# Performance work log

Hardware: AMD Instinct MI355X
Metric: run time of the kernel (lower is better)

## Reference

```python
import jax, jax.numpy as jnp
import numpy as np

B, T, C = 2, 2048, 1024
H, D = 16, 64
F = 4096
EPS = 1e-5


def _layernorm(x, scale, shift):
    mean = jnp.mean(x, axis=-1, keepdims=True)
    var = jnp.mean((x - mean) ** 2, axis=-1, keepdims=True)  # unbiased=False
    return scale * (x - mean) * jax.lax.rsqrt(var + EPS) + shift


def setup_inputs() -> dict:
    key = jax.random.key(0)
    ks = jax.random.split(key, 16)
    s = lambda k, shape, fan_in: jax.random.normal(k, shape, jnp.float32) * (1.0 / np.sqrt(fan_in))
    return {
        "x": jax.random.normal(ks[0], (B, T, C), jnp.float32),
        # weights stored [in, out] so y = x @ W + b (same math as torch Linear)
        "Wq": s(ks[1], (C, H * D), C), "bq": jnp.zeros((H * D,), jnp.float32),
        "Wk": s(ks[2], (C, H * D), C), "bk": jnp.zeros((H * D,), jnp.float32),
        "Wv": s(ks[3], (C, H * D), C), "bv": jnp.zeros((H * D,), jnp.float32),
        "Wo": s(ks[4], (H * D, C), H * D), "bo": jnp.zeros((C,), jnp.float32),
        "W1": s(ks[5], (C, F), C), "b1": jnp.zeros((F,), jnp.float32),
        "W2": s(ks[6], (F, C), F), "b2": jnp.zeros((C,), jnp.float32),
        "ln1_scale": jnp.ones((C,), jnp.float32), "ln1_shift": jnp.zeros((C,), jnp.float32),
        "ln2_scale": jnp.ones((C,), jnp.float32), "ln2_shift": jnp.zeros((C,), jnp.float32),
    }


def reference(x, Wq, bq, Wk, bk, Wv, bv, Wo, bo, W1, b1, W2, b2,
              ln1_scale, ln1_shift, ln2_scale, ln2_shift):
    b, t, c = x.shape
    # --- attention sub-block ---
    h = _layernorm(x, ln1_scale, ln1_shift)
    q = (h @ Wq + bq).reshape(b, t, H, D)
    k = (h @ Wk + bk).reshape(b, t, H, D)
    v = (h @ Wv + bv).reshape(b, t, H, D)
    scores = jnp.einsum('bqhd,bkhd->bhqk', q, k)  # [B,H,T,T]
    causal = jnp.tril(jnp.ones((t, t), dtype=bool))
    scores = jnp.where(causal, scores, -jnp.inf)
    attn = jax.nn.softmax(scores / np.sqrt(D), axis=-1)
    ctx = jnp.einsum('bhqk,bkhd->bqhd', attn, v).reshape(b, t, H * D)
    x = x + (ctx @ Wo + bo)  # drop_rate=0 -> dropout is identity
    # --- MLP sub-block ---
    h = _layernorm(x, ln2_scale, ln2_shift)
    h = jax.nn.gelu(h @ W1 + b1, approximate=False)
    x = x + (h @ W2 + b2)
    return x
```

## Files before the change

### kernel.cpp

```cpp
#include <hip/hip_runtime.h>
#include <hip/hip_bf16.h>
#include <stdint.h>

#define B_ 2
#define T_ 2048
#define C_ 1024
#define H_ 16
#define D_ 64
#define F_ 4096
#define M_ (B_*T_)

typedef unsigned short ushort_t;
typedef __attribute__((ext_vector_type(8))) short short8;
typedef __attribute__((ext_vector_type(4))) float f32x4;

__device__ __forceinline__ float bf2f(ushort_t u) {
    union { unsigned u; float f; } c; c.u = ((unsigned)u) << 16; return c.f;
}
__device__ __forceinline__ ushort_t f2bf(float f) {
    union { float f; unsigned u; } c; c.f = f;
    unsigned u = c.u;
    unsigned r = (u + 0x7FFFu + ((u >> 16) & 1u)) >> 16;
    return (ushort_t)r;
}

__device__ __forceinline__ void async16(void* lds, const void* g) {
    __builtin_amdgcn_global_load_lds(
        (const __attribute__((address_space(1))) unsigned int*)(uintptr_t)g,
        (__attribute__((address_space(3))) unsigned int*)(uintptr_t)lds,
        16, 0, 0);
}

__global__ void transpose_cast_k(const float* __restrict__ in, ushort_t* __restrict__ out,
                                 int R, int C) {
    __shared__ ushort_t tile[32][33];
    int tx = threadIdx.x, ty = threadIdx.y;
    int x = blockIdx.x * 32 + tx;
    int y0 = blockIdx.y * 32;
#pragma unroll
    for (int i = 0; i < 32; i += 8)
        tile[ty + i][tx] = f2bf(in[(size_t)(y0 + ty + i) * C + x]);
    __syncthreads();
    int x2 = y0 + tx;
    int y2 = blockIdx.x * 32;
#pragma unroll
    for (int i = 0; i < 32; i += 8)
        out[(size_t)(y2 + ty + i) * R + x2] = tile[tx][ty + i];
}

__global__ void transpose_bf_k(const ushort_t* __restrict__ in, ushort_t* __restrict__ out,
                               int R, int C) {
    __shared__ ushort_t tile[32][33];
    int tx = threadIdx.x, ty = threadIdx.y;
    int x = blockIdx.x * 32 + tx;
    int y0 = blockIdx.y * 32;
#pragma unroll
    for (int i = 0; i < 32; i += 8)
        tile[ty + i][tx] = in[(size_t)(y0 + ty + i) * C + x];
    __syncthreads();
    int x2 = y0 + tx;
    int y2 = blockIdx.x * 32;
#pragma unroll
    for (int i = 0; i < 32; i += 8)
        out[(size_t)(y2 + ty + i) * R + x2] = tile[tx][ty + i];
}

__global__ __launch_bounds__(256) void ln_kernel(const float* __restrict__ xin,
                                                 const float* __restrict__ scale_p,
                                                 const float* __restrict__ shift_p,
                                                 ushort_t* __restrict__ out) {
    int row = blockIdx.x, t = threadIdx.x;
    int wv = t >> 6, lane = t & 63;
    const float* xr = xin + (size_t)row * 1024 + t * 4;
    float4 v = *(const float4*)xr;
    float f[4] = {v.x, v.y, v.z, v.w};
    float s = f[0] + f[1] + f[2] + f[3];
    float q = f[0]*f[0] + f[1]*f[1] + f[2]*f[2] + f[3]*f[3];
#pragma unroll
    for (int off = 1; off < 64; off <<= 1) {
        s += __shfl_xor(s, off, 64);
        q += __shfl_xor(q, off, 64);
    }
    __shared__ float sh_s[4], sh_q[4];
    if (lane == 0) { sh_s[wv] = s; sh_q[wv] = q; }
    __syncthreads();
    float S = sh_s[0] + sh_s[1] + sh_s[2] + sh_s[3];
    float Q = sh_q[0] + sh_q[1] + sh_q[2] + sh_q[3];
    float mean = S * (1.0f / 1024.0f);
    float var = Q * (1.0f / 1024.0f) - mean * mean;
    float rstd = rsqrtf(var + 1e-5f);
    float4 scv = *(const float4*)(scale_p + t * 4);
    float4 shv = *(const float4*)(shift_p + t * 4);
    ushort4 o;
    o.x = f2bf((f[0] - mean) * rstd * scv.x + shv.x);
    o.y = f2bf((f[1] - mean) * rstd * scv.y + shv.y);
    o.z = f2bf((f[2] - mean) * rstd * scv.z + shv.z);
    o.w = f2bf((f[3] - mean) * rstd * scv.w + shv.w);
    *(ushort4*)(out + (size_t)row * 1024 + t * 4) = o;
}

template <int MT, int EPI>
__global__ __launch_bounds__(256) void gemm_bt(const ushort_t* __restrict__ A,
                                               const ushort_t* __restrict__ Bt,
                                               const float* __restrict__ b0,
                                               const float* __restrict__ b1,
                                               const float* __restrict__ b2,
                                               const float* __restrict__ res,
                                               void* __restrict__ out0,
                                               void* __restrict__ out1,
                                               void* __restrict__ out2,
                                               int M, int N, int K) {
    __shared__ ushort_t As[32 * MT * 32];
    __shared__ ushort_t Bs[128 * 32];
    const int t = threadIdx.x;
    const int wv = t >> 6, lane = t & 63, lo = lane & 15, hi = lane >> 4;
    const int wr = wv >> 1, wc = wv & 1;
    const int mb = blockIdx.y, nb = blockIdx.x;

    f32x4 acc[MT][4];
#pragma unroll
    for (int i = 0; i < MT; ++i)
#pragma unroll
        for (int j = 0; j < 4; ++j) acc[i][j] = (f32x4){0.f, 0.f, 0.f, 0.f};

    for (int k0 = 0; k0 < K; k0 += 32) {
#pragma unroll
        for (int i = 0; i < MT / 2; ++i) {
            int c = i * 256 + t;
            int row = c >> 2, kc = c & 3;
            async16((char*)As + (size_t)(i * 256 + wv * 64) * 16,
                    A + (size_t)(mb * 32 * MT + row) * K + k0 + kc * 8);
        }
#pragma unroll
        for (int i = 0; i < 2; ++i) {
            int c = i * 256 + t;
            int row = c >> 2, kc = c & 3;
            async16((char*)Bs + (size_t)(i * 256 + wv * 64) * 16,
                    Bt + (size_t)(nb * 128 + row) * K + k0 + kc * 8);
        }
        __syncthreads();

        short8 af[MT], bfr[4];
#pragma unroll
        for (int mi = 0; mi < MT; ++mi)
            af[mi] = *(const short8*)(As + (wr * 16 * MT + mi * 16 + lo) * 32 + hi * 8);
#pragma unroll
        for (int ni = 0; ni < 4; ++ni)
            bfr[ni] = *(const short8*)(Bs + (wc * 64 + ni * 16 + lo) * 32 + hi * 8);
#pragma unroll
        for (int mi = 0; mi < MT; ++mi)
#pragma unroll
            for (int ni = 0; ni < 4; ++ni)
                acc[mi][ni] = __builtin_amdgcn_mfma_f32_16x16x32_bf16(
                    af[mi], bfr[ni], acc[mi][ni], 0, 0, 0);
        __syncthreads();
    }

#pragma unroll
    for (int ni = 0; ni < 4; ++ni) {
        int n = nb * 128 + wc * 64 + ni * 16 + lo;
        float bn;
        ushort_t* obf = nullptr;
        int coln = n;
        if (EPI == 3) {
            int seg = n >> 10; coln = n & 1023;
            bn = (seg == 0 ? b0 : seg == 1 ? b1 : b2)[coln];
            obf = (ushort_t*)(seg == 0 ? out0 : seg == 1 ? out1 : out2);
        } else {
            bn = b0[n];
        }
#pragma unroll
        for (int mi = 0; mi < MT; ++mi) {
#pragma unroll
            for (int r = 0; r < 4; ++r) {
                int m = mb * 32 * MT + wr * 16 * MT + mi * 16 + 4 * hi + r;
                float v = acc[mi][ni][r] + bn;
                if (EPI == 1) {
                    size_t idx = (size_t)m * N + n;
                    ((float*)out0)[idx] = v + res[idx];
                } else if (EPI == 2) {
                    v = 0.5f * v * (1.0f + erff(v * 0.70710678118654752f));
                    ((ushort_t*)out0)[(size_t)m * N + n] = f2bf(v);
                } else {
                    obf[(size_t)m * 1024 + coln] = f2bf(v);
                }
            }
        }
    }
}

__global__ __launch_bounds__(256) void attn_kernel(const ushort_t* __restrict__ q,
                                                   const ushort_t* __restrict__ k,
                                                   const ushort_t* __restrict__ vt,
                                                   ushort_t* __restrict__ ctx) {
    __shared__ ushort_t Ks[64 * 64];
    __shared__ ushort_t VTs[64 * 64];
    __shared__ ushort_t Ps[4][16 * 88];

    const int t = threadIdx.x;
    const int wv = t >> 6, lane = t & 63, lo = lane & 15, hi = lane >> 4;
    const int qb = (int)gridDim.x - 1 - (int)blockIdx.x;
    const int bh = blockIdx.y, b = bh >> 4, h = bh & 15;
    const int q0 = qb * 64;
    const size_t headoff = (size_t)h * 64;
    const size_t rowbase = (size_t)b * T_ * 1024;
    const ushort_t* vbase = vt + headoff * (size_t)M_ + (size_t)b * T_;

    const ushort_t* qptr = q + rowbase + (size_t)(q0 + wv * 16 + lo) * 1024 + headoff;
    short8 qf0 = *(const short8*)(qptr + hi * 8);
    short8 qf1 = *(const short8*)(qptr + 32 + hi * 8);

    float m_r[4], l_r[4];
    f32x4 o_acc[4];
#pragma unroll
    for (int r = 0; r < 4; ++r) { m_r[r] = -1e30f; l_r[r] = 0.f; }
#pragma unroll
    for (int dt = 0; dt < 4; ++dt) o_acc[dt] = (f32x4){0.f, 0.f, 0.f, 0.f};

    for (int kt = 0; kt <= qb; ++kt) {
        const int k0 = kt * 64;
#pragma unroll
        for (int i = 0; i < 2; ++i) {
            int c = i * 256 + t;
            int row = c >> 3, c8 = c & 7;
            int g = c8 ^ (row & 7);
            async16((char*)Ks + (size_t)(i * 256 + wv * 64) * 16,
                    k + rowbase + (size_t)(k0 + row) * 1024 + headoff + g * 8);
            async16((char*)VTs + (size_t)(i * 256 + wv * 64) * 16,
                    vbase + (size_t)row * M_ + k0 + g * 8);
        }
        __syncthreads();

        const int cmax = (kt == qb) ? wv : 3;
        f32x4 sacc[4];
#pragma unroll
        for (int kt16 = 0; kt16 < 4; ++kt16) {
            if (kt16 <= cmax) {
                int row = kt16 * 16 + lo, sw = row & 7;
                short8 kf0 = *(const short8*)(Ks + row * 64 + (hi ^ sw) * 8);
                short8 kf1 = *(const short8*)(Ks + row * 64 + ((4 + hi) ^ sw) * 8);
                f32x4 z = (f32x4){0.f, 0.f, 0.f, 0.f};
                z = __builtin_amdgcn_mfma_f32_16x16x32_bf16(qf0, kf0, z, 0, 0, 0);
                z = __builtin_amdgcn_mfma_f32_16x16x32_bf16(qf1, kf1, z, 0, 0, 0);
#pragma unroll
                for (int r = 0; r < 4; ++r) sacc[kt16][r] = z[r] * 0.125f;
            } else {
                sacc[kt16] = (f32x4){-1e30f, -1e30f, -1e30f, -1e30f};
            }
        }
        if (kt == qb) {
            int key = k0 + wv * 16 + lo;
#pragma unroll
            for (int r = 0; r < 4; ++r) {
                int qrow = q0 + wv * 16 + 4 * hi + r;
                if (key > qrow) sacc[wv][r] = -1e30f;
            }
        }

        ushort_t* Pw = Ps[wv];
#pragma unroll
        for (int r = 0; r < 4; ++r) {
            float mx = fmaxf(fmaxf(sacc[0][r], sacc[1][r]), fmaxf(sacc[2][r], sacc[3][r]));
#pragma unroll
            for (int off = 1; off < 16; off <<= 1) mx = fmaxf(mx, __shfl_xor(mx, off, 64));
            float mnew = fmaxf(m_r[r], mx);
            float alpha = __expf(m_r[r] - mnew);
            m_r[r] = mnew;
            float rs = 0.f;
#pragma unroll
            for (int kt16 = 0; kt16 < 4; ++kt16) {
                float p = __expf(sacc[kt16][r] - mnew);
                rs += p;
                Pw[(4 * hi + r) * 88 + kt16 * 16 + lo] = f2bf(p);
            }
#pragma unroll
            for (int off = 1; off < 16; off <<= 1) rs += __shfl_xor(rs, off, 64);
            l_r[r] = l_r[r] * alpha + rs;
#pragma unroll
            for (int dt = 0; dt < 4; ++dt) o_acc[dt][r] *= alpha;
        }
        __syncthreads();

        short8 pf0 = *(const short8*)(Pw + lo * 88 + hi * 8);
        short8 pf1 = *(const short8*)(Pw + lo * 88 + 32 + hi * 8);
#pragma unroll
        for (int dt = 0; dt < 4; ++dt) {
            int row = dt * 16 + lo, sw = row & 7;
            short8 vf0 = *(const short8*)(VTs + row * 64 + (hi ^ sw) * 8);
            short8 vf1 = *(const short8*)(VTs + row * 64 + ((4 + hi) ^ sw) * 8);
            o_acc[dt] = __builtin_amdgcn_mfma_f32_16x16x32_bf16(pf0, vf0, o_acc[dt], 0, 0, 0);
            o_acc[dt] = __builtin_amdgcn_mfma_f32_16x16x32_bf16(pf1, vf1, o_acc[dt], 0, 0, 0);
        }
        __syncthreads();
    }

#pragma unroll
    for (int r = 0; r < 4; ++r) {
        float inv = 1.0f / l_r[r];
        size_t row = rowbase + (size_t)(q0 + wv * 16 + 4 * hi + r) * 1024 + headoff;
#pragma unroll
        for (int dt = 0; dt < 4; ++dt)
            ctx[row + dt * 16 + lo] = f2bf(o_acc[dt][r] * inv);
    }
}

extern "C" void kernel_launch(void* const* d_in, const int* in_sizes, int n_in,
                              void* d_out, int out_size, void* d_ws, size_t ws_size,
                              hipStream_t stream) {
    (void)in_sizes; (void)n_in; (void)out_size; (void)ws_size;
    const float* x    = (const float*)d_in[0];
    const float* Wq   = (const float*)d_in[1];
    const float* bq   = (const float*)d_in[2];
    const float* Wk   = (const float*)d_in[3];
    const float* bk   = (const float*)d_in[4];
    const float* Wv   = (const float*)d_in[5];
    const float* bv   = (const float*)d_in[6];
    const float* Wo   = (const float*)d_in[7];
    const float* bo   = (const float*)d_in[8];
    const float* W1   = (const float*)d_in[9];
    const float* b1   = (const float*)d_in[10];
    const float* W2   = (const float*)d_in[11];
    const float* b2   = (const float*)d_in[12];
    const float* ln1s = (const float*)d_in[13];
    const float* ln1b = (const float*)d_in[14];
    const float* ln2s = (const float*)d_in[15];
    const float* ln2b = (const float*)d_in[16];

    char* ws = (char*)d_ws;
    const size_t MB = 1024 * 1024;
    ushort_t* wqkv = (ushort_t*)(ws + 0 * MB);
    ushort_t* wtq  = (ushort_t*)(ws + 0 * MB);
    ushort_t* wtk  = (ushort_t*)(ws + 2 * MB);
    ushort_t* wtv  = (ushort_t*)(ws + 4 * MB);
    ushort_t* wto  = (ushort_t*)(ws + 6 * MB);
    ushort_t* wt1  = (ushort_t*)(ws + 8 * MB);
    ushort_t* wt2  = (ushort_t*)(ws + 16 * MB);
    ushort_t* hbuf = (ushort_t*)(ws + 24 * MB);
    ushort_t* qb_  = (ushort_t*)(ws + 32 * MB);
    ushort_t* kb_  = (ushort_t*)(ws + 40 * MB);
    ushort_t* vb_  = (ushort_t*)(ws + 48 * MB);
    ushort_t* ctx  = (ushort_t*)(ws + 56 * MB);
    ushort_t* hid  = (ushort_t*)(ws + 32 * MB);
    float*    x1   = (float*)(ws + 64 * MB);
    ushort_t* vtb  = (ushort_t*)(ws + 64 * MB);

    dim3 tb(32, 8);
    transpose_cast_k<<<dim3(32, 32), tb, 0, stream>>>(Wq, wtq, 1024, 1024);
    transpose_cast_k<<<dim3(32, 32), tb, 0, stream>>>(Wk, wtk, 1024, 1024);
    transpose_cast_k<<<dim3(32, 32), tb, 0, stream>>>(Wv, wtv, 1024, 1024);
    transpose_cast_k<<<dim3(32, 32), tb, 0, stream>>>(Wo, wto, 1024, 1024);
    transpose_cast_k<<<dim3(128, 32), tb, 0, stream>>>(W1, wt1, 1024, 4096);
    transpose_cast_k<<<dim3(32, 128), tb, 0, stream>>>(W2, wt2, 4096, 1024);

    ln_kernel<<<4096, 256, 0, stream>>>(x, ln1s, ln1b, hbuf);

    gemm_bt<4, 3><<<dim3(24, 32), 256, 0, stream>>>(hbuf, wqkv, bq, bk, bv, nullptr,
                                                    qb_, kb_, vb_, 4096, 3072, 1024);

    transpose_bf_k<<<dim3(32, 128), tb, 0, stream>>>(vb_, vtb, 4096, 1024);

    attn_kernel<<<dim3(32, 32), 256, 0, stream>>>(qb_, kb_, vtb, ctx);

    gemm_bt<2, 1><<<dim3(8, 64), 256, 0, stream>>>(ctx, wto, bo, nullptr, nullptr, x,
                                                   x1, nullptr, nullptr, 4096, 1024, 1024);

    ln_kernel<<<4096, 256, 0, stream>>>(x1, ln2s, ln2b, hbuf);

    gemm_bt<4, 2><<<dim3(32, 32), 256, 0, stream>>>(hbuf, wt1, b1, nullptr, nullptr, nullptr,
                                                    hid, nullptr, nullptr, 4096, 4096, 1024);

    gemm_bt<2, 1><<<dim3(8, 64), 256, 0, stream>>>(hid, wt2, b2, nullptr, nullptr, x1,
                                                   (float*)d_out, nullptr, nullptr, 4096, 1024, 4096);
}
```

Measured before the change: 487.9 us.

## Double-buffer K/V tiles and process 128 query rows per attention block

Each attention block now covers 128 query rows as two 64-row groups, so every staged K/V tile is reused by both groups. K and V^T use double-buffered LDS with the next tile prefetched during compute, which drops two of the three barriers per iteration. The QK product is transposed so each lane holds a full query row, giving lane-local max and sum reductions with fewer shuffles, and the softmax scale is folded into exp2. The costs are half as many blocks (less parallelism, possible causal load imbalance), more registers and more LDS.

```diff
diff --git a/kernel.cpp b/kernel.cpp
--- a/kernel.cpp
+++ b/kernel.cpp
@@ -23,6 +23,8 @@
     unsigned r = (u + 0x7FFFu + ((u >> 16) & 1u)) >> 16;
     return (ushort_t)r;
 }
+
+__device__ __forceinline__ float fexp2(float x) { return __builtin_amdgcn_exp2f(x); }
 
 __device__ __forceinline__ void async16(void* lds, const void* g) {
     __builtin_amdgcn_global_load_lds(
@@ -193,114 +195,156 @@
                                                    const ushort_t* __restrict__ k,
                                                    const ushort_t* __restrict__ vt,
                                                    ushort_t* __restrict__ ctx) {
-    __shared__ ushort_t Ks[64 * 64];
-    __shared__ ushort_t VTs[64 * 64];
-    __shared__ ushort_t Ps[4][16 * 88];
+    __shared__ ushort_t Ks[2][64 * 64];
+    __shared__ ushort_t VTs[2][64 * 64];
+    __shared__ ushort_t Ps[8][16 * 72];
 
     const int t = threadIdx.x;
     const int wv = t >> 6, lane = t & 63, lo = lane & 15, hi = lane >> 4;
     const int qb = (int)gridDim.x - 1 - (int)blockIdx.x;
     const int bh = blockIdx.y, b = bh >> 4, h = bh & 15;
-    const int q0 = qb * 64;
+    const int q0 = qb * 128;
     const size_t headoff = (size_t)h * 64;
     const size_t rowbase = (size_t)b * T_ * 1024;
     const ushort_t* vbase = vt + headoff * (size_t)M_ + (size_t)b * T_;
 
-    const ushort_t* qptr = q + rowbase + (size_t)(q0 + wv * 16 + lo) * 1024 + headoff;
-    short8 qf0 = *(const short8*)(qptr + hi * 8);
-    short8 qf1 = *(const short8*)(qptr + 32 + hi * 8);
-
-    float m_r[4], l_r[4];
-    f32x4 o_acc[4];
-#pragma unroll
-    for (int r = 0; r < 4; ++r) { m_r[r] = -1e30f; l_r[r] = 0.f; }
-#pragma unroll
-    for (int dt = 0; dt < 4; ++dt) o_acc[dt] = (f32x4){0.f, 0.f, 0.f, 0.f};
-
-    for (int kt = 0; kt <= qb; ++kt) {
+    short8 qf[2][2];
+#pragma unroll
+    for (int g = 0; g < 2; ++g) {
+        const ushort_t* qp = q + rowbase + (size_t)(q0 + g * 64 + wv * 16 + lo) * 1024 + headoff;
+        qf[g][0] = *(const short8*)(qp + hi * 8);
+        qf[g][1] = *(const short8*)(qp + 32 + hi * 8);
+    }
+
+    float m_g[2], l_g[2];
+    f32x4 o_acc[2][4];
+#pragma unroll
+    for (int g = 0; g < 2; ++g) {
+        m_g[g] = -1e30f; l_g[g] = 0.f;
+#pragma unroll
+        for (int dt = 0; dt < 4; ++dt) o_acc[g][dt] = (f32x4){0.f, 0.f, 0.f, 0.f};
+    }
+
+    const int ktmax = 2 * qb + 1;
+    const float SC = 0.18033688011112042f;
+
+    auto stage = [&](int bb, int kt) {
         const int k0 = kt * 64;
 #pragma unroll
         for (int i = 0; i < 2; ++i) {
             int c = i * 256 + t;
             int row = c >> 3, c8 = c & 7;
-            int g = c8 ^ (row & 7);
-            async16((char*)Ks + (size_t)(i * 256 + wv * 64) * 16,
-                    k + rowbase + (size_t)(k0 + row) * 1024 + headoff + g * 8);
-            async16((char*)VTs + (size_t)(i * 256 + wv * 64) * 16,
-                    vbase + (size_t)row * M_ + k0 + g * 8);
-        }
+            int gsw = c8 ^ (row & 7);
+            async16((char*)&Ks[bb][0] + (size_t)(i * 256 + wv * 64) * 16,
+                    k + rowbase + (size_t)(k0 + row) * 1024 + headoff + gsw * 8);
+            async16((char*)&VTs[bb][0] + (size_t)(i * 256 + wv * 64) * 16,
+                    vbase + (size_t)row * M_ + k0 + gsw * 8);
+        }
+    };
+
+    stage(0, 0);
+    for (int kt = 0; kt <= ktmax; ++kt) {
+        const int bb = kt & 1;
+        const int k0 = kt * 64;
         __syncthreads();
-
-        const int cmax = (kt == qb) ? wv : 3;
-        f32x4 sacc[4];
-#pragma unroll
-        for (int kt16 = 0; kt16 < 4; ++kt16) {
-            if (kt16 <= cmax) {
-                int row = kt16 * 16 + lo, sw = row & 7;
-                short8 kf0 = *(const short8*)(Ks + row * 64 + (hi ^ sw) * 8);
-                short8 kf1 = *(const short8*)(Ks + row * 64 + ((4 + hi) ^ sw) * 8);
-                f32x4 z = (f32x4){0.f, 0.f, 0.f, 0.f};
-                z = __builtin_amdgcn_mfma_f32_16x16x32_bf16(qf0, kf0, z, 0, 0, 0);
-                z = __builtin_amdgcn_mfma_f32_16x16x32_bf16(qf1, kf1, z, 0, 0, 0);
-#pragma unroll
-                for (int r = 0; r < 4; ++r) sacc[kt16][r] = z[r] * 0.125f;
-            } else {
-                sacc[kt16] = (f32x4){-1e30f, -1e30f, -1e30f, -1e30f};
+        if (kt < ktmax) stage(bb ^ 1, kt + 1);
+
+        short8 pf[2][2];
+        int any_g[2];
+#pragma unroll
+        for (int g = 0; g < 2; ++g) {
+            const int qg0 = q0 + g * 64 + wv * 16;
+            const int diff = qg0 - k0;
+            any_g[g] = (diff >= 0);
+            if (!any_g[g]) continue;
+            const int cmax = diff >= 48 ? 3 : (diff >> 4);
+
+            f32x4 sacc[4];
+#pragma unroll
+            for (int kt16 = 0; kt16 < 4; ++kt16) {
+                if (kt16 <= cmax) {
+                    int row = kt16 * 16 + lo, sw = row & 7;
+                    short8 kf0 = *(const short8*)(&Ks[bb][0] + row * 64 + (hi ^ sw) * 8);
+                    short8 kf1 = *(const short8*)(&Ks[bb][0] + row * 64 + ((4 + hi) ^ sw) * 8);
+                    f32x4 z = (f32x4){0.f, 0.f, 0.f, 0.f};
+                    z = __builtin_amdgcn_mfma_f32_16x16x32_bf16(kf0, qf[g][0], z, 0, 0, 0);
+                    z = __builtin_amdgcn_mfma_f32_16x16x32_bf16(kf1, qf[g][1], z, 0, 0, 0);
+#pragma unroll
+                    for (int r = 0; r < 4; ++r) sacc[kt16][r] = z[r] * SC;
+                } else {
+                    sacc[kt16] = (f32x4){-1e30f, -1e30f, -1e30f, -1e30f};
+                }
             }
-        }
-        if (kt == qb) {
-            int key = k0 + wv * 16 + lo;
+            if (diff < 64) {
+                const int qrow = qg0 + lo;
+#pragma unroll
+                for (int r = 0; r < 4; ++r) {
+                    int key = k0 + cmax * 16 + 4 * hi + r;
+                    if (key > qrow) sacc[cmax][r] = -1e30f;
+                }
+            }
+
+            float mx = -1e30f;
+#pragma unroll
+            for (int kt16 = 0; kt16 < 4; ++kt16)
+#pragma unroll
+                for (int r = 0; r < 4; ++r) mx = fmaxf(mx, sacc[kt16][r]);
+            mx = fmaxf(mx, __shfl_xor(mx, 16, 64));
+            mx = fmaxf(mx, __shfl_xor(mx, 32, 64));
+            float mnew = fmaxf(m_g[g], mx);
+            float alpha = fexp2(m_g[g] - mnew);
+            m_g[g] = mnew;
+
+            ushort_t* Pw = Ps[wv * 2 + g];
+            float rs = 0.f;
+#pragma unroll
+            for (int kt16 = 0; kt16 < 4; ++kt16)
+#pragma unroll
+                for (int r = 0; r < 4; ++r) {
+                    float p = fexp2(sacc[kt16][r] - mnew);
+                    rs += p;
+                    Pw[lo * 72 + kt16 * 16 + 4 * hi + r] = f2bf(p);
+                }
+            rs += __shfl_xor(rs, 16, 64);
+            rs += __shfl_xor(rs, 32, 64);
+            l_g[g] = l_g[g] * alpha + rs;
+
 #pragma unroll
             for (int r = 0; r < 4; ++r) {
-                int qrow = q0 + wv * 16 + 4 * hi + r;
-                if (key > qrow) sacc[wv][r] = -1e30f;
+                float ab = __shfl(alpha, 4 * hi + r, 64);
+#pragma unroll
+                for (int dt = 0; dt < 4; ++dt) o_acc[g][dt][r] *= ab;
             }
-        }
-
-        ushort_t* Pw = Ps[wv];
-#pragma unroll
-        for (int r = 0; r < 4; ++r) {
-            float mx = fmaxf(fmaxf(sacc[0][r], sacc[1][r]), fmaxf(sacc[2][r], sacc[3][r]));
-#pragma unroll
-            for (int off = 1; off < 16; off <<= 1) mx = fmaxf(mx, __shfl_xor(mx, off, 64));
-            float mnew = fmaxf(m_r[r], mx);
-            float alpha = __expf(m_r[r] - mnew);
-            m_r[r] = mnew;
-            float rs = 0.f;
-#pragma unroll
-            for (int kt16 = 0; kt16 < 4; ++kt16) {
-                float p = __expf(sacc[kt16][r] - mnew);
-                rs += p;
-                Pw[(4 * hi + r) * 88 + kt16 * 16 + lo] = f2bf(p);
-            }
-#pragma unroll
-            for (int off = 1; off < 16; off <<= 1) rs += __shfl_xor(rs, off, 64);
-            l_r[r] = l_r[r] * alpha + rs;
-#pragma unroll
-            for (int dt = 0; dt < 4; ++dt) o_acc[dt][r] *= alpha;
-        }
-        __syncthreads();
-
-        short8 pf0 = *(const short8*)(Pw + lo * 88 + hi * 8);
-        short8 pf1 = *(const short8*)(Pw + lo * 88 + 32 + hi * 8);
+
+            pf[g][0] = *(const short8*)(Pw + lo * 72 + hi * 8);
+            pf[g][1] = *(const short8*)(Pw + lo * 72 + 32 + hi * 8);
+        }
+
 #pragma unroll
         for (int dt = 0; dt < 4; ++dt) {
             int row = dt * 16 + lo, sw = row & 7;
-            short8 vf0 = *(const short8*)(VTs + row * 64 + (hi ^ sw) * 8);
-            short8 vf1 = *(const short8*)(VTs + row * 64 + ((4 + hi) ^ sw) * 8);
-            o_acc[dt] = __builtin_amdgcn_mfma_f32_16x16x32_bf16(pf0, vf0, o_acc[dt], 0, 0, 0);
-            o_acc[dt] = __builtin_amdgcn_mfma_f32_16x16x32_bf16(pf1, vf1, o_acc[dt], 0, 0, 0);
-        }
-        __syncthreads();
-    }
-
-#pragma unroll
-    for (int r = 0; r < 4; ++r) {
-        float inv = 1.0f / l_r[r];
-        size_t row = rowbase + (size_t)(q0 + wv * 16 + 4 * hi + r) * 1024 + headoff;
-#pragma unroll
-        for (int dt = 0; dt < 4; ++dt)
-            ctx[row + dt * 16 + lo] = f2bf(o_acc[dt][r] * inv);
+            short8 vf0 = *(const short8*)(&VTs[bb][0] + row * 64 + (hi ^ sw) * 8);
+            short8 vf1 = *(const short8*)(&VTs[bb][0] + row * 64 + ((4 + hi) ^ sw) * 8);
+#pragma unroll
+            for (int g = 0; g < 2; ++g) {
+                if (!any_g[g]) continue;
+                o_acc[g][dt] = __builtin_amdgcn_mfma_f32_16x16x32_bf16(pf[g][0], vf0, o_acc[g][dt], 0, 0, 0);
+                o_acc[g][dt] = __builtin_amdgcn_mfma_f32_16x16x32_bf16(pf[g][1], vf1, o_acc[g][dt], 0, 0, 0);
+            }
+        }
+    }
+
+#pragma unroll
+    for (int g = 0; g < 2; ++g) {
+#pragma unroll
+        for (int r = 0; r < 4; ++r) {
+            float lb = __shfl(l_g[g], 4 * hi + r, 64);
+            float inv = 1.0f / lb;
+            size_t row = rowbase + (size_t)(q0 + g * 64 + wv * 16 + 4 * hi + r) * 1024 + headoff;
+#pragma unroll
+            for (int dt = 0; dt < 4; ++dt)
+                ctx[row + dt * 16 + lo] = f2bf(o_acc[g][dt][r] * inv);
+        }
     }
 }
 
@@ -359,7 +403,7 @@
 
     transpose_bf_k<<<dim3(32, 128), tb, 0, stream>>>(vb_, vtb, 4096, 1024);
 
-    attn_kernel<<<dim3(32, 32), 256, 0, stream>>>(qb_, kb_, vtb, ctx);
+    attn_kernel<<<dim3(16, 32), 256, 0, stream>>>(qb_, kb_, vtb, ctx);
 
     gemm_bt<2, 1><<<dim3(8, 64), 256, 0, stream>>>(ctx, wto, bo, nullptr, nullptr, x,
                                                    x1, nullptr, nullptr, 4096, 1024, 1024);
```

After: 456.9 us. 1.07x faster.
